# Kernel optimization log

Measured on AMD Instinct MI355X. Metric: run time of the kernel, lower is better.

The kernel has to match this reference:

```python
import jax, jax.numpy as jnp
import numpy as np

D_MODEL = 1024
D_HIDDEN = 4096
N_EXPERTS = 8
N_TOKENS = 4096


def setup_inputs() -> dict:
    key = jax.random.key(0)
    ks = jax.random.split(key, 7)
    s = 0.02
    return {
        "x": jax.random.normal(ks[0], (N_TOKENS, D_MODEL), dtype=jnp.float32),
        "gate_w": jax.random.normal(ks[1], (N_EXPERTS, D_MODEL), dtype=jnp.float32) * s,
        "gate_b": jnp.zeros((N_EXPERTS,), dtype=jnp.float32),
        "w1": jax.random.normal(ks[2], (N_EXPERTS, D_MODEL, D_HIDDEN), dtype=jnp.float32) * s,
        "b1": jnp.zeros((N_EXPERTS, D_HIDDEN), dtype=jnp.float32),
        "w2": jax.random.normal(ks[3], (N_EXPERTS, D_HIDDEN, D_MODEL), dtype=jnp.float32) * s,
        "b2": jnp.zeros((N_EXPERTS, D_MODEL), dtype=jnp.float32),
    }


def reference(x, gate_w, gate_b, w1, b1, w2, b2):
    # gate: softmax over expert logits, hard top-1 routing (no prob weighting,
    # matching the torch module which writes the raw expert output back)
    gate_logits = x @ gate_w.T + gate_b                      # [N, E]
    gate_probs = jax.nn.softmax(gate_logits, axis=-1)
    top_expert = jnp.argmax(gate_probs, axis=-1)             # [N] int

    # dense all-expert MLP, then one-hot select (vectorized top-1 MoE)
    h = jax.nn.relu(jnp.einsum('nd,edh->neh', x, w1) + b1[None])  # [N, E, Dh]
    y = jnp.einsum('neh,ehd->ned', h, w2) + b2[None]              # [N, E, D]
    onehot = jax.nn.one_hot(top_expert, N_EXPERTS, dtype=x.dtype)  # [N, E]
    out = jnp.einsum('ned,ne->nd', y, onehot)                      # [N, D]
    return out
```

## Files before the change

kernel.cpp:

```cpp
#include <hip/hip_runtime.h>
#include <hip/hip_bf16.h>

#define NT 4096
#define DM 1024
#define DH 4096
#define NE 8

#define BM 128
#define BN 128
#define BK 32
#define MAXT 40
#define MAXROWS 5120
#define KSPL2 2
#define BKP 40
#define G1B (8 * 4 * MAXT)

typedef short bf16x8 __attribute__((ext_vector_type(8)));
typedef float f32x4 __attribute__((ext_vector_type(4)));
typedef float f4 __attribute__((ext_vector_type(4)));

#define MI_COUNTS 0
#define MI_POFF   16
#define MI_NTILES 32
#define MI_TILEE  48
#define MI_TILER  112
#define MI_TILES0 176

#define O_BUCKET 1024ull
#define O_XB  (O_BUCKET + (size_t)NE * NT * 4)
#define O_H   (O_XB + (size_t)NT * DM * 2)
#define O_W1T (O_H + (size_t)MAXROWS * DH * 2)
#define O_W2T (O_W1T + (size_t)NE * DM * DH * 2)
#define WS_NEED (O_W2T + (size_t)NE * DH * DM * 2)
#define O_P   O_W1T

static __device__ __forceinline__ unsigned short f2bf(float f) {
  union { __hip_bfloat16 h; unsigned short u; } cv;
  cv.h = __float2bfloat16(f);
  return cv.u;
}

static __device__ __forceinline__ void gload16(const void* g, void* l) {
  __builtin_amdgcn_global_load_lds(
      (const __attribute__((address_space(1))) void*)g,
      (__attribute__((address_space(3))) void*)l, 16, 0, 0);
}

static __device__ __forceinline__ void convert_v4(
    const float* __restrict__ S, __hip_bfloat16* __restrict__ D, int N,
    int KTcnt, int kglob0, int nglob0, char* smem) {
  auto Ls = reinterpret_cast<__hip_bfloat16(*)[72]>(smem);
  const int tid = threadIdx.x;
  const int c4 = tid & 15, rk = tid >> 4;
  const float* src = S + (size_t)(kglob0 + rk * 4) * N + nglob0 + c4 * 4;
  f4 v[4];
#pragma unroll
  for (int j = 0; j < 4; ++j) v[j] = *(const f4*)(src + (size_t)j * N);
#pragma unroll
  for (int i = 0; i < 4; ++i) {
    ushort4 w;
    w.x = f2bf(v[0][i]); w.y = f2bf(v[1][i]);
    w.z = f2bf(v[2][i]); w.w = f2bf(v[3][i]);
    *(ushort4*)&Ls[c4 * 4 + i][rk * 4] = w;
  }
  __syncthreads();
  const int r = tid >> 2, q = tid & 3;
  const int nt = nglob0 >> 7;
  const int npr = (nglob0 & 64) + r;
#pragma unroll
  for (int u = 0; u < 2; ++u) {
    const int g = q * 2 + u;
    const int kt = (kglob0 >> 5) + (g >> 2);
    uint4 w = *(const uint4*)&Ls[r][g * 8];
    *(uint4*)(D + ((size_t)nt * KTcnt + kt) * 4096 + npr * 32 + (g & 3) * 8) =
        w;
  }
}

static __device__ __forceinline__ void gate_body(
    const float* __restrict__ x, const float* __restrict__ gw,
    const float* __restrict__ gb, int* __restrict__ counts,
    int* __restrict__ bucket, __hip_bfloat16* __restrict__ xb, int bid) {
  const int tid = threadIdx.x;
  const int wid = tid >> 6;
  const int lane = tid & 63;
  const int t = bid * 4 + wid;

  const f4* xrow = (const f4*)(x + (size_t)t * DM);
  ushort4* xbrow = (ushort4*)(xb + (size_t)t * DM);

  double part[NE];
#pragma unroll
  for (int e = 0; e < NE; ++e) part[e] = 0.0;

#pragma unroll
  for (int q = 0; q < 4; ++q) {
    f4 v = xrow[q * 64 + lane];
    ushort4 s;
    s.x = f2bf(v[0]); s.y = f2bf(v[1]); s.z = f2bf(v[2]); s.w = f2bf(v[3]);
    xbrow[q * 64 + lane] = s;
#pragma unroll
    for (int e = 0; e < NE; ++e) {
      f4 w = ((const f4*)(gw + (size_t)e * DM))[q * 64 + lane];
      part[e] += (double)v[0] * w[0] + (double)v[1] * w[1] +
                 (double)v[2] * w[2] + (double)v[3] * w[3];
    }
  }
#pragma unroll
  for (int off = 32; off; off >>= 1) {
#pragma unroll
    for (int e = 0; e < NE; ++e) part[e] += __shfl_down(part[e], off);
  }
  if (lane == 0) {
    double best = part[0] + (double)gb[0];
    int bi = 0;
#pragma unroll
    for (int e = 1; e < NE; ++e) {
      double le = part[e] + (double)gb[e];
      if (le > best) { best = le; bi = e; }
    }
    int pos = atomicAdd(&counts[bi], 1);
    bucket[bi * NT + pos] = t;
  }
}

__global__ __launch_bounds__(256) void gate_route_kernel(
    const float* __restrict__ x, const float* __restrict__ gw,
    const float* __restrict__ gb, int* __restrict__ counts,
    int* __restrict__ bucket, __hip_bfloat16* __restrict__ xb) {
  gate_body(x, gw, gb, counts, bucket, xb, blockIdx.x);
}

__global__ __launch_bounds__(256) void cw1_kernel(
    const float* __restrict__ w1, __hip_bfloat16* __restrict__ w1t) {
  __shared__ __align__(16) char smem[9216];
  const int id = blockIdx.x;
  const int e = id >> 10;
  const int rem = id & 1023;
  const int kglob0 = (rem >> 6) * 64;
  const int nglob0 = (rem & 63) * 64;
  convert_v4(w1 + (size_t)e * DM * DH, w1t + (size_t)e * DM * DH, DH,
             DM / 32, kglob0, nglob0, smem);
}

__global__ void prefix_kernel(int* __restrict__ meta, int* __restrict__ bucket) {
  if (threadIdx.x == 0) {
    int r = 0, nt = 0;
    for (int e = 0; e < NE; ++e) {
      meta[MI_POFF + e] = r;
      const int cnt = meta[MI_COUNTS + e];
      const int T = (cnt + BM - 1) / BM;
      for (int j = 0; j < T; ++j) {
        meta[MI_TILEE + nt] = e;
        meta[MI_TILER + nt] = r + j * BM;
        meta[MI_TILES0 + nt] = j * BM;
        ++nt;
      }
      r += T * BM;
    }
    meta[MI_POFF + NE] = r;
    meta[MI_NTILES] = nt;
  }
  __syncthreads();
  for (int e = 0; e < NE; ++e) {
    const int cnt = meta[MI_COUNTS + e];
    if (cnt == 0) continue;
    const int padTo = ((cnt + BM - 1) / BM) * BM;
    const int last = bucket[e * NT + cnt - 1];
    for (int i = cnt + threadIdx.x; i < padTo; i += blockDim.x)
      bucket[e * NT + i] = last;
  }
}

template <int MODE>
static __device__ __forceinline__ void gemm_body(
    char* smem, int b, const __hip_bfloat16* __restrict__ A,
    const __hip_bfloat16* __restrict__ B, const float* __restrict__ biasAll,
    const int* __restrict__ meta, const int* __restrict__ bucket,
    void* __restrict__ Out) {
  auto As = reinterpret_cast<__hip_bfloat16(*)[BM][BK]>(smem);
  auto Bs = reinterpret_cast<__hip_bfloat16(*)[BN][BK]>(smem + 16384);

  const int xcd = b & 7;
  const int idx = b >> 3;
  int tile, ntile, kq;
  if (MODE == 0) {
    const int grp = idx / MAXT;
    tile = idx - grp * MAXT;
    ntile = xcd * 4 + grp;
    kq = 0;
  } else {
    const int grp = idx / MAXT;
    tile = idx - grp * MAXT;
    const int np = xcd * 2 + grp;
    ntile = np >> 1;
    kq = np & 1;
  }
  if (tile >= meta[MI_NTILES]) return;

  const int e = meta[MI_TILEE + tile];
  const int row0 = meta[MI_TILER + tile];
  const int s0 = meta[MI_TILES0 + tile];
  const int n0 = ntile * BN;
  const int KTM = (MODE == 0) ? 32 : 64;
  const int kbase = (MODE == 0) ? 0 : kq * (DH / KSPL2);
  const int NT1 = (MODE == 0) ? (DH / 128) : (DM / 128);
  const int KTcnt = (MODE == 0) ? (DM / 32) : (DH / 32);
  const int ktb = (MODE == 0) ? 0 : kq * 64;

  const int tid = threadIdx.x;
  const int lane = tid & 63;
  const int wid = tid >> 6;
  const int lr = lane >> 2, lc = lane & 3;

  const __hip_bfloat16 *aP0, *aP1;
  if (MODE == 0) {
    aP0 = A + (size_t)bucket[e * NT + s0 + 32 * wid + lr] * DM + lc * 8;
    aP1 = A + (size_t)bucket[e * NT + s0 + 32 * wid + 16 + lr] * DM + lc * 8;
  } else {
    aP0 = A + (size_t)(row0 + 32 * wid + lr) * DH + kbase + lc * 8;
    aP1 = A + (size_t)(row0 + 32 * wid + 16 + lr) * DH + kbase + lc * 8;
  }
  const __hip_bfloat16* bP0 =
      B + (((size_t)e * NT1 + ntile) * KTcnt + ktb) * 4096 + wid * 1024 +
      lane * 8;
  const __hip_bfloat16* bP1 = bP0 + 512;

  const int wm = (wid >> 1) * 64, wn = (wid & 1) * 64;
  const int fr = lane & 15, ks = lane >> 4;

  f32x4 acc[4][4];
#pragma unroll
  for (int m = 0; m < 4; ++m)
#pragma unroll
    for (int n = 0; n < 4; ++n) acc[m][n] = (f32x4){0.f, 0.f, 0.f, 0.f};

#define STAGE(bf, kt)                                              \
  do {                                                             \
    gload16(aP0 + (size_t)(kt) * BK, &As[bf][32 * wid][0]);        \
    gload16(aP1 + (size_t)(kt) * BK, &As[bf][32 * wid + 16][0]);   \
    gload16(bP0 + (size_t)(kt) * 4096, &Bs[bf][32 * wid][0]);      \
    gload16(bP1 + (size_t)(kt) * 4096, &Bs[bf][32 * wid + 16][0]); \
  } while (0)

  STAGE(0, 0);
  __syncthreads();

  for (int kt = 0; kt < KTM; ++kt) {
    const int buf = kt & 1;
    if (kt + 1 < KTM) STAGE(buf ^ 1, kt + 1);
    bf16x8 afr[4], bfr[4];
#pragma unroll
    for (int m = 0; m < 4; ++m)
      afr[m] = *(const bf16x8*)&As[buf][wm + m * 16 + fr][ks * 8];
#pragma unroll
    for (int n = 0; n < 4; ++n)
      bfr[n] = *(const bf16x8*)&Bs[buf][wn + n * 16 + fr][ks * 8];
#pragma unroll
    for (int m = 0; m < 4; ++m)
#pragma unroll
      for (int n = 0; n < 4; ++n)
        acc[m][n] = __builtin_amdgcn_mfma_f32_16x16x32_bf16(afr[m], bfr[n],
                                                            acc[m][n], 0, 0, 0);
    __syncthreads();
  }
#undef STAGE

  if (MODE == 0) {
    const float* bias = biasAll + (size_t)e * DH;
    __hip_bfloat16* Hout = (__hip_bfloat16*)Out;
#pragma unroll
    for (int m = 0; m < 4; ++m)
#pragma unroll
      for (int r = 0; r < 4; ++r) {
        const int row = wm + m * 16 + ks * 4 + r;
        __hip_bfloat16* orow = Hout + (size_t)(row0 + row) * DH;
#pragma unroll
        for (int n = 0; n < 4; ++n) {
          const int col = n0 + wn + n * 16 + fr;
          float v = acc[m][n][r] + bias[col];
          orow[col] = __float2bfloat16(v > 0.f ? v : 0.f);
        }
      }
  } else {
    float* Pout = (float*)Out + (size_t)kq * MAXROWS * DM;
#pragma unroll
    for (int m = 0; m < 4; ++m)
#pragma unroll
      for (int r = 0; r < 4; ++r) {
        const int row = wm + m * 16 + ks * 4 + r;
        float* orow = Pout + (size_t)(row0 + row) * DM;
#pragma unroll
        for (int n = 0; n < 4; ++n) {
          const int col = n0 + wn + n * 16 + fr;
          orow[col] = acc[m][n][r];
        }
      }
  }
}

__global__ __launch_bounds__(256, 2) void gemm1_cw2_kernel(
    const __hip_bfloat16* __restrict__ xb, const __hip_bfloat16* __restrict__ w1t,
    const float* __restrict__ b1, const int* __restrict__ meta,
    const int* __restrict__ bucket, __hip_bfloat16* __restrict__ h,
    const float* __restrict__ w2, __hip_bfloat16* __restrict__ w2t) {
  __shared__ __align__(16) char smem[32768];
  const int bid = blockIdx.x;
  if (bid < G1B) {
    gemm_body<0>(smem, bid, xb, w1t, b1, meta, bucket, (void*)h);
    return;
  }
  const int id = bid - G1B;
  const int e = id >> 10;
  const int rem = id & 1023;
  const int kglob0 = (rem >> 4) * 64;
  const int nglob0 = (rem & 15) * 64;
  convert_v4(w2 + (size_t)e * DH * DM, w2t + (size_t)e * DH * DM, DM,
             DH / 32, kglob0, nglob0, smem);
}

__global__ __launch_bounds__(256, 2) void gemm2_kernel(
    const __hip_bfloat16* __restrict__ h, const __hip_bfloat16* __restrict__ w2t,
    const int* __restrict__ meta, const int* __restrict__ bucket,
    float* __restrict__ P) {
  __shared__ __align__(16) char smem[32768];
  gemm_body<1>(smem, blockIdx.x, h, w2t, nullptr, meta, bucket, (void*)P);
}

__global__ __launch_bounds__(256) void reduce_out_kernel(
    const float* __restrict__ P, const float* __restrict__ b2,
    const int* __restrict__ meta, const int* __restrict__ bucket,
    float* __restrict__ out) {
  const int gs = blockIdx.x;
  if (gs >= meta[MI_POFF + NE]) return;
  int e = 0;
#pragma unroll
  for (int i = 1; i < NE; ++i) e = (gs >= meta[MI_POFF + i]) ? i : e;
  const int i = gs - meta[MI_POFF + e];
  if (i >= meta[MI_COUNTS + e]) return;
  const int tok = bucket[e * NT + i];
  const int c = threadIdx.x * 4;
  float4 v = *(const float4*)(P + (size_t)gs * DM + c);
#pragma unroll
  for (int q = 1; q < KSPL2; ++q) {
    float4 p = *(const float4*)(P + ((size_t)q * MAXROWS + gs) * DM + c);
    v.x += p.x; v.y += p.y; v.z += p.z; v.w += p.w;
  }
  float4 b = *(const float4*)(b2 + (size_t)e * DM + c);
  v.x += b.x; v.y += b.y; v.z += b.z; v.w += b.w;
  *(float4*)(out + (size_t)tok * DM + c) = v;
}

template <bool RELU_BF16>
__global__ __launch_bounds__(256, 2) void moe_gemm_fallback(
    const __hip_bfloat16* __restrict__ Aall, int lda,
    const float* __restrict__ Ball, int K, int N,
    const float* __restrict__ biasAll, const int* __restrict__ counts,
    const int* __restrict__ bucket, void* __restrict__ Out, int ldo) {
  const int e = blockIdx.z;
  const int cnt = counts[e];
  const int m0 = blockIdx.y * BM;
  if (m0 >= cnt) return;
  const int n0 = blockIdx.x * BN;

  const float* Bp = Ball + (size_t)e * K * N;
  const float* bias = biasAll + (size_t)e * N;
  const int* buck = bucket + e * NT;

  __shared__ __align__(16) __hip_bfloat16 As[2][BM][BKP];
  __shared__ __align__(16) __hip_bfloat16 Bs[2][BN][BKP];

  const int tid = threadIdx.x;
  const int lane = tid & 63;
  const int wid = tid >> 6;
  const int wm = (wid >> 1) * 64;
  const int wn = (wid & 1) * 64;
  const int fr = lane & 15;
  const int ks = lane >> 4;

  const int ar = tid >> 1;
  const int ah = tid & 1;
  const int atok = buck[min(m0 + ar, cnt - 1)];
  const __hip_bfloat16* aptr = Aall + (size_t)atok * lda + ah * 16;

  const int bc = tid & 31;
  const int bk0 = (tid >> 5) * 4;

  f32x4 acc[4][4];
#pragma unroll
  for (int m = 0; m < 4; ++m)
#pragma unroll
    for (int n = 0; n < 4; ++n) acc[m][n] = (f32x4){0.f, 0.f, 0.f, 0.f};

  const int KTf = K / BK;
  uint4 ra0, ra1;
  float rb[4][4];

  {
    const uint4* p = (const uint4*)(aptr);
    ra0 = p[0]; ra1 = p[1];
    const float* bbase = Bp + (size_t)bk0 * N + n0 + bc;
#pragma unroll
    for (int i = 0; i < 4; ++i)
#pragma unroll
      for (int j = 0; j < 4; ++j) rb[i][j] = bbase[(size_t)i * N + 32 * j];
  }
  {
    *(uint4*)&As[0][ar][ah * 16] = ra0;
    *(uint4*)&As[0][ar][ah * 16 + 8] = ra1;
#pragma unroll
    for (int j = 0; j < 4; ++j) {
      ushort4 w;
      w.x = f2bf(rb[0][j]); w.y = f2bf(rb[1][j]);
      w.z = f2bf(rb[2][j]); w.w = f2bf(rb[3][j]);
      *(ushort4*)&Bs[0][bc + 32 * j][bk0] = w;
    }
  }
  __syncthreads();

  for (int kt = 0; kt < KTf; ++kt) {
    const int buf = kt & 1;
    if (kt + 1 < KTf) {
      const uint4* p = (const uint4*)(aptr + (size_t)(kt + 1) * BK);
      ra0 = p[0]; ra1 = p[1];
      const float* bbase = Bp + (size_t)((kt + 1) * BK + bk0) * N + n0 + bc;
#pragma unroll
      for (int i = 0; i < 4; ++i)
#pragma unroll
        for (int j = 0; j < 4; ++j) rb[i][j] = bbase[(size_t)i * N + 32 * j];
    }

    bf16x8 afr[4], bfr[4];
#pragma unroll
    for (int m = 0; m < 4; ++m)
      afr[m] = *(const bf16x8*)&As[buf][wm + m * 16 + fr][ks * 8];
#pragma unroll
    for (int n = 0; n < 4; ++n)
      bfr[n] = *(const bf16x8*)&Bs[buf][wn + n * 16 + fr][ks * 8];
#pragma unroll
    for (int m = 0; m < 4; ++m)
#pragma unroll
      for (int n = 0; n < 4; ++n)
        acc[m][n] = __builtin_amdgcn_mfma_f32_16x16x32_bf16(afr[m], bfr[n],
                                                            acc[m][n], 0, 0, 0);

    __syncthreads();
    if (kt + 1 < KTf) {
      *(uint4*)&As[buf ^ 1][ar][ah * 16] = ra0;
      *(uint4*)&As[buf ^ 1][ar][ah * 16 + 8] = ra1;
#pragma unroll
      for (int j = 0; j < 4; ++j) {
        ushort4 w;
        w.x = f2bf(rb[0][j]); w.y = f2bf(rb[1][j]);
        w.z = f2bf(rb[2][j]); w.w = f2bf(rb[3][j]);
        *(uint2*)&Bs[buf ^ 1][bc + 32 * j][bk0] = *(uint2*)&w;
      }
      __syncthreads();
    }
  }

  float* outF = (float*)Out;
  __hip_bfloat16* outB = (__hip_bfloat16*)Out;
#pragma unroll
  for (int m = 0; m < 4; ++m) {
#pragma unroll
    for (int r = 0; r < 4; ++r) {
      const int row = wm + m * 16 + ks * 4 + r;
      const int slot = m0 + row;
      if (slot < cnt) {
        const int tok = buck[slot];
#pragma unroll
        for (int n = 0; n < 4; ++n) {
          const int col = n0 + wn + n * 16 + fr;
          float v = acc[m][n][r] + bias[col];
          if (RELU_BF16) {
            v = v > 0.f ? v : 0.f;
            outB[(size_t)tok * ldo + col] = __float2bfloat16(v);
          } else {
            outF[(size_t)tok * ldo + col] = v;
          }
        }
      }
    }
  }
}

extern "C" void kernel_launch(void* const* d_in, const int* in_sizes, int n_in,
                              void* d_out, int out_size, void* d_ws,
                              size_t ws_size, hipStream_t stream) {
  const float* x = (const float*)d_in[0];
  const float* gw = (const float*)d_in[1];
  const float* gb = (const float*)d_in[2];
  const float* w1 = (const float*)d_in[3];
  const float* b1 = (const float*)d_in[4];
  const float* w2 = (const float*)d_in[5];
  const float* b2 = (const float*)d_in[6];
  (void)in_sizes; (void)n_in; (void)out_size;

  char* ws = (char*)d_ws;
  int* meta = (int*)ws;
  int* counts = meta + MI_COUNTS;
  int* bucket = (int*)(ws + O_BUCKET);
  __hip_bfloat16* xb = (__hip_bfloat16*)(ws + O_XB);
  __hip_bfloat16* h = (__hip_bfloat16*)(ws + O_H);

  hipMemsetAsync(ws, 0, 1024, stream);

  if (ws_size >= WS_NEED) {
    __hip_bfloat16* w1t = (__hip_bfloat16*)(ws + O_W1T);
    __hip_bfloat16* w2t = (__hip_bfloat16*)(ws + O_W2T);
    float* P = (float*)(ws + O_P);

    gate_route_kernel<<<NT / 4, 256, 0, stream>>>(x, gw, gb, counts, bucket,
                                                  xb);
    cw1_kernel<<<8192, 256, 0, stream>>>(w1, w1t);
    prefix_kernel<<<1, 256, 0, stream>>>(meta, bucket);
    gemm1_cw2_kernel<<<G1B + 8192, 256, 0, stream>>>(
        xb, w1t, b1, meta, bucket, h, w2, w2t);
    gemm2_kernel<<<8 * 2 * MAXT, 256, 0, stream>>>(h, w2t, meta, bucket, P);
    reduce_out_kernel<<<MAXROWS, 256, 0, stream>>>(P, b2, meta, bucket,
                                                   (float*)d_out);
  } else {
    gate_route_kernel<<<NT / 4, 256, 0, stream>>>(x, gw, gb, counts, bucket,
                                                  xb);
    dim3 g1(DH / BN, NT / BM, NE);
    moe_gemm_fallback<true><<<g1, 256, 0, stream>>>(
        xb, DM, w1, DM, DH, b1, counts, bucket, (void*)h, DH);
    dim3 g2(DM / BN, NT / BM, NE);
    moe_gemm_fallback<false><<<g2, 256, 0, stream>>>(
        h, DH, w2, DH, DM, b2, counts, bucket, d_out, DM);
  }
}
```

Before: 264.1 us.

## Fuse w1 fp32-to-bf16 conversion into gemm1 B-tile loading

Drops the separate cw1 pass that converted and retiled w1 into bf16 in workspace. gemm1 now reads fp32 w1 directly, converts it to bf16 in registers, and writes it into a padded shared-memory B tile, with loads prefetched two k-steps ahead. This removes a full read and write of w1 plus one kernel launch. In exchange, each w1 element is reread and reconverted by every row tile of its expert, and the fp32 loads are strided scalar loads rather than 16-byte direct-to-LDS copies.

Result: faster. 251.4 us (-4.8%).

```diff
diff --git a/kernel.cpp b/kernel.cpp
--- a/kernel.cpp
+++ b/kernel.cpp
@@ -129,18 +129,6 @@
     const float* __restrict__ gb, int* __restrict__ counts,
     int* __restrict__ bucket, __hip_bfloat16* __restrict__ xb) {
   gate_body(x, gw, gb, counts, bucket, xb, blockIdx.x);
-}
-
-__global__ __launch_bounds__(256) void cw1_kernel(
-    const float* __restrict__ w1, __hip_bfloat16* __restrict__ w1t) {
-  __shared__ __align__(16) char smem[9216];
-  const int id = blockIdx.x;
-  const int e = id >> 10;
-  const int rem = id & 1023;
-  const int kglob0 = (rem >> 6) * 64;
-  const int nglob0 = (rem & 63) * 64;
-  convert_v4(w1 + (size_t)e * DM * DH, w1t + (size_t)e * DM * DH, DH,
-             DM / 32, kglob0, nglob0, smem);
 }
 
 __global__ void prefix_kernel(int* __restrict__ meta, int* __restrict__ bucket) {
@@ -172,58 +160,159 @@
   }
 }
 
-template <int MODE>
-static __device__ __forceinline__ void gemm_body(
+static __device__ __forceinline__ void gemm1_body_f32b(
     char* smem, int b, const __hip_bfloat16* __restrict__ A,
-    const __hip_bfloat16* __restrict__ B, const float* __restrict__ biasAll,
+    const float* __restrict__ w1, const float* __restrict__ biasAll,
     const int* __restrict__ meta, const int* __restrict__ bucket,
-    void* __restrict__ Out) {
+    __hip_bfloat16* __restrict__ Hout) {
   auto As = reinterpret_cast<__hip_bfloat16(*)[BM][BK]>(smem);
-  auto Bs = reinterpret_cast<__hip_bfloat16(*)[BN][BK]>(smem + 16384);
+  auto Bs = reinterpret_cast<__hip_bfloat16(*)[BN][BKP]>(smem + 16384);
 
   const int xcd = b & 7;
   const int idx = b >> 3;
-  int tile, ntile, kq;
-  if (MODE == 0) {
-    const int grp = idx / MAXT;
-    tile = idx - grp * MAXT;
-    ntile = xcd * 4 + grp;
-    kq = 0;
-  } else {
-    const int grp = idx / MAXT;
-    tile = idx - grp * MAXT;
-    const int np = xcd * 2 + grp;
-    ntile = np >> 1;
-    kq = np & 1;
-  }
+  const int grp = idx / MAXT;
+  const int tile = idx - grp * MAXT;
+  const int ntile = xcd * 4 + grp;
   if (tile >= meta[MI_NTILES]) return;
 
   const int e = meta[MI_TILEE + tile];
   const int row0 = meta[MI_TILER + tile];
   const int s0 = meta[MI_TILES0 + tile];
   const int n0 = ntile * BN;
-  const int KTM = (MODE == 0) ? 32 : 64;
-  const int kbase = (MODE == 0) ? 0 : kq * (DH / KSPL2);
-  const int NT1 = (MODE == 0) ? (DH / 128) : (DM / 128);
-  const int KTcnt = (MODE == 0) ? (DM / 32) : (DH / 32);
-  const int ktb = (MODE == 0) ? 0 : kq * 64;
 
   const int tid = threadIdx.x;
   const int lane = tid & 63;
   const int wid = tid >> 6;
   const int lr = lane >> 2, lc = lane & 3;
 
-  const __hip_bfloat16 *aP0, *aP1;
-  if (MODE == 0) {
-    aP0 = A + (size_t)bucket[e * NT + s0 + 32 * wid + lr] * DM + lc * 8;
-    aP1 = A + (size_t)bucket[e * NT + s0 + 32 * wid + 16 + lr] * DM + lc * 8;
-  } else {
-    aP0 = A + (size_t)(row0 + 32 * wid + lr) * DH + kbase + lc * 8;
-    aP1 = A + (size_t)(row0 + 32 * wid + 16 + lr) * DH + kbase + lc * 8;
-  }
+  const __hip_bfloat16* aP0 =
+      A + (size_t)bucket[e * NT + s0 + 32 * wid + lr] * DM + lc * 8;
+  const __hip_bfloat16* aP1 =
+      A + (size_t)bucket[e * NT + s0 + 32 * wid + 16 + lr] * DM + lc * 8;
+
+  const int bc = tid & 31;
+  const int bk0 = (tid >> 5) * 4;
+  const float* Bp = w1 + (size_t)e * DM * DH + n0 + bc;
+
+  const int wm = (wid >> 1) * 64, wn = (wid & 1) * 64;
+  const int fr = lane & 15, ks = lane >> 4;
+
+  f32x4 acc[4][4];
+#pragma unroll
+  for (int m = 0; m < 4; ++m)
+#pragma unroll
+    for (int n = 0; n < 4; ++n) acc[m][n] = (f32x4){0.f, 0.f, 0.f, 0.f};
+
+  float rb[4][4];
+
+#define BLOAD(kt)                                                     \
+  do {                                                                \
+    const float* bbase = Bp + (size_t)((kt) * BK + bk0) * DH;         \
+    _Pragma("unroll") for (int i = 0; i < 4; ++i)                     \
+        _Pragma("unroll") for (int j = 0; j < 4; ++j)                 \
+            rb[i][j] = bbase[(size_t)i * DH + 32 * j];                \
+  } while (0)
+
+#define BWRITE(bf)                                                    \
+  do {                                                                \
+    _Pragma("unroll") for (int j = 0; j < 4; ++j) {                   \
+      ushort4 w;                                                      \
+      w.x = f2bf(rb[0][j]); w.y = f2bf(rb[1][j]);                     \
+      w.z = f2bf(rb[2][j]); w.w = f2bf(rb[3][j]);                     \
+      *(ushort4*)&Bs[bf][bc + 32 * j][bk0] = w;                       \
+    }                                                                 \
+  } while (0)
+
+#define ASTAGE(bf, kt)                                                \
+  do {                                                                \
+    gload16(aP0 + (size_t)(kt) * BK, &As[bf][32 * wid][0]);           \
+    gload16(aP1 + (size_t)(kt) * BK, &As[bf][32 * wid + 16][0]);      \
+  } while (0)
+
+  BLOAD(0);
+  ASTAGE(0, 0);
+  BWRITE(0);
+  if (1 < 32) BLOAD(1);
+  __syncthreads();
+
+  for (int kt = 0; kt < 32; ++kt) {
+    const int buf = kt & 1;
+    if (kt + 1 < 32) ASTAGE(buf ^ 1, kt + 1);
+    bf16x8 afr[4], bfr[4];
+#pragma unroll
+    for (int m = 0; m < 4; ++m)
+      afr[m] = *(const bf16x8*)&As[buf][wm + m * 16 + fr][ks * 8];
+#pragma unroll
+    for (int n = 0; n < 4; ++n)
+      bfr[n] = *(const bf16x8*)&Bs[buf][wn + n * 16 + fr][ks * 8];
+#pragma unroll
+    for (int m = 0; m < 4; ++m)
+#pragma unroll
+      for (int n = 0; n < 4; ++n)
+        acc[m][n] = __builtin_amdgcn_mfma_f32_16x16x32_bf16(afr[m], bfr[n],
+                                                            acc[m][n], 0, 0, 0);
+    __syncthreads();
+    if (kt + 1 < 32) {
+      BWRITE(buf ^ 1);
+      if (kt + 2 < 32) BLOAD(kt + 2);
+      __syncthreads();
+    }
+  }
+#undef BLOAD
+#undef BWRITE
+#undef ASTAGE
+
+  const float* bias = biasAll + (size_t)e * DH;
+#pragma unroll
+  for (int m = 0; m < 4; ++m)
+#pragma unroll
+    for (int r = 0; r < 4; ++r) {
+      const int row = wm + m * 16 + ks * 4 + r;
+      __hip_bfloat16* orow = Hout + (size_t)(row0 + row) * DH;
+#pragma unroll
+      for (int n = 0; n < 4; ++n) {
+        const int col = n0 + wn + n * 16 + fr;
+        float v = acc[m][n][r] + bias[col];
+        orow[col] = __float2bfloat16(v > 0.f ? v : 0.f);
+      }
+    }
+}
+
+static __device__ __forceinline__ void gemm2_body(
+    char* smem, int b, const __hip_bfloat16* __restrict__ A,
+    const __hip_bfloat16* __restrict__ B, const int* __restrict__ meta,
+    float* __restrict__ Pout0) {
+  auto As = reinterpret_cast<__hip_bfloat16(*)[BM][BK]>(smem);
+  auto Bs = reinterpret_cast<__hip_bfloat16(*)[BN][BK]>(smem + 16384);
+
+  const int xcd = b & 7;
+  const int idx = b >> 3;
+  const int grp = idx / MAXT;
+  const int tile = idx - grp * MAXT;
+  const int np = xcd * 2 + grp;
+  const int ntile = np >> 1;
+  const int kq = np & 1;
+  if (tile >= meta[MI_NTILES]) return;
+
+  const int e = meta[MI_TILEE + tile];
+  const int row0 = meta[MI_TILER + tile];
+  const int n0 = ntile * BN;
+  const int kbase = kq * (DH / KSPL2);
+  const int KTcnt = DH / 32;
+  const int ktb = kq * 64;
+
+  const int tid = threadIdx.x;
+  const int lane = tid & 63;
+  const int wid = tid >> 6;
+  const int lr = lane >> 2, lc = lane & 3;
+
+  const __hip_bfloat16* aP0 =
+      A + (size_t)(row0 + 32 * wid + lr) * DH + kbase + lc * 8;
+  const __hip_bfloat16* aP1 =
+      A + (size_t)(row0 + 32 * wid + 16 + lr) * DH + kbase + lc * 8;
   const __hip_bfloat16* bP0 =
-      B + (((size_t)e * NT1 + ntile) * KTcnt + ktb) * 4096 + wid * 1024 +
-      lane * 8;
+      B + (((size_t)e * (DM / 128) + ntile) * KTcnt + ktb) * 4096 +
+      wid * 1024 + lane * 8;
   const __hip_bfloat16* bP1 = bP0 + 512;
 
   const int wm = (wid >> 1) * 64, wn = (wid & 1) * 64;
@@ -246,9 +335,9 @@
   STAGE(0, 0);
   __syncthreads();
 
-  for (int kt = 0; kt < KTM; ++kt) {
+  for (int kt = 0; kt < 64; ++kt) {
     const int buf = kt & 1;
-    if (kt + 1 < KTM) STAGE(buf ^ 1, kt + 1);
+    if (kt + 1 < 64) STAGE(buf ^ 1, kt + 1);
     bf16x8 afr[4], bfr[4];
 #pragma unroll
     for (int m = 0; m < 4; ++m)
@@ -266,48 +355,30 @@
   }
 #undef STAGE
 
-  if (MODE == 0) {
-    const float* bias = biasAll + (size_t)e * DH;
-    __hip_bfloat16* Hout = (__hip_bfloat16*)Out;
-#pragma unroll
-    for (int m = 0; m < 4; ++m)
-#pragma unroll
-      for (int r = 0; r < 4; ++r) {
-        const int row = wm + m * 16 + ks * 4 + r;
-        __hip_bfloat16* orow = Hout + (size_t)(row0 + row) * DH;
-#pragma unroll
-        for (int n = 0; n < 4; ++n) {
-          const int col = n0 + wn + n * 16 + fr;
-          float v = acc[m][n][r] + bias[col];
-          orow[col] = __float2bfloat16(v > 0.f ? v : 0.f);
-        }
+  float* Pout = Pout0 + (size_t)kq * MAXROWS * DM;
+#pragma unroll
+  for (int m = 0; m < 4; ++m)
+#pragma unroll
+    for (int r = 0; r < 4; ++r) {
+      const int row = wm + m * 16 + ks * 4 + r;
+      float* orow = Pout + (size_t)(row0 + row) * DM;
+#pragma unroll
+      for (int n = 0; n < 4; ++n) {
+        const int col = n0 + wn + n * 16 + fr;
+        orow[col] = acc[m][n][r];
       }
-  } else {
-    float* Pout = (float*)Out + (size_t)kq * MAXROWS * DM;
-#pragma unroll
-    for (int m = 0; m < 4; ++m)
-#pragma unroll
-      for (int r = 0; r < 4; ++r) {
-        const int row = wm + m * 16 + ks * 4 + r;
-        float* orow = Pout + (size_t)(row0 + row) * DM;
-#pragma unroll
-        for (int n = 0; n < 4; ++n) {
-          const int col = n0 + wn + n * 16 + fr;
-          orow[col] = acc[m][n][r];
-        }
-      }
-  }
-}
-
-__global__ __launch_bounds__(256, 2) void gemm1_cw2_kernel(
-    const __hip_bfloat16* __restrict__ xb, const __hip_bfloat16* __restrict__ w1t,
+    }
+}
+
+__global__ __launch_bounds__(256, 2) void gemm1f_cw2_kernel(
+    const __hip_bfloat16* __restrict__ xb, const float* __restrict__ w1,
     const float* __restrict__ b1, const int* __restrict__ meta,
     const int* __restrict__ bucket, __hip_bfloat16* __restrict__ h,
     const float* __restrict__ w2, __hip_bfloat16* __restrict__ w2t) {
-  __shared__ __align__(16) char smem[32768];
+  __shared__ __align__(16) char smem[36864];
   const int bid = blockIdx.x;
   if (bid < G1B) {
-    gemm_body<0>(smem, bid, xb, w1t, b1, meta, bucket, (void*)h);
+    gemm1_body_f32b(smem, bid, xb, w1, b1, meta, bucket, h);
     return;
   }
   const int id = bid - G1B;
@@ -321,10 +392,9 @@
 
 __global__ __launch_bounds__(256, 2) void gemm2_kernel(
     const __hip_bfloat16* __restrict__ h, const __hip_bfloat16* __restrict__ w2t,
-    const int* __restrict__ meta, const int* __restrict__ bucket,
-    float* __restrict__ P) {
+    const int* __restrict__ meta, float* __restrict__ P) {
   __shared__ __align__(16) char smem[32768];
-  gemm_body<1>(smem, blockIdx.x, h, w2t, nullptr, meta, bucket, (void*)P);
+  gemm2_body(smem, blockIdx.x, h, w2t, meta, P);
 }
 
 __global__ __launch_bounds__(256) void reduce_out_kernel(
@@ -453,7 +523,7 @@
         ushort4 w;
         w.x = f2bf(rb[0][j]); w.y = f2bf(rb[1][j]);
         w.z = f2bf(rb[2][j]); w.w = f2bf(rb[3][j]);
-        *(uint2*)&Bs[buf ^ 1][bc + 32 * j][bk0] = *(uint2*)&w;
+        *(ushort4*)&Bs[buf ^ 1][bc + 32 * j][bk0] = w;
       }
       __syncthreads();
     }
@@ -507,17 +577,15 @@
   hipMemsetAsync(ws, 0, 1024, stream);
 
   if (ws_size >= WS_NEED) {
-    __hip_bfloat16* w1t = (__hip_bfloat16*)(ws + O_W1T);
     __hip_bfloat16* w2t = (__hip_bfloat16*)(ws + O_W2T);
     float* P = (float*)(ws + O_P);
 
     gate_route_kernel<<<NT / 4, 256, 0, stream>>>(x, gw, gb, counts, bucket,
                                                   xb);
-    cw1_kernel<<<8192, 256, 0, stream>>>(w1, w1t);
     prefix_kernel<<<1, 256, 0, stream>>>(meta, bucket);
-    gemm1_cw2_kernel<<<G1B + 8192, 256, 0, stream>>>(
-        xb, w1t, b1, meta, bucket, h, w2, w2t);
-    gemm2_kernel<<<8 * 2 * MAXT, 256, 0, stream>>>(h, w2t, meta, bucket, P);
+    gemm1f_cw2_kernel<<<G1B + 8192, 256, 0, stream>>>(
+        xb, w1, b1, meta, bucket, h, w2, w2t);
+    gemm2_kernel<<<8 * 2 * MAXT, 256, 0, stream>>>(h, w2t, meta, P);
     reduce_out_kernel<<<MAXROWS, 256, 0, stream>>>(P, b2, meta, bucket,
                                                    (float*)d_out);
   } else {
```
